# Optimization experiments

Measured on AMD Instinct MI355X. Metric: run time of the kernel, lower is better.

## Reference

```python
import jax, jax.numpy as jnp
import numpy as np

N_NODES = 50000
N_EDGES = 800000
IN_DIM = 64
HEADS = 8
OUT_DIM = 8
CLAMP = 5.0


def _xavier(key, shape, fan_in, fan_out):
    std = float(np.sqrt(2.0 / (fan_in + fan_out)))
    return jax.random.normal(key, shape, dtype=jnp.float32) * std


def setup_inputs() -> dict:
    key = jax.random.key(0)
    ks = jax.random.split(key, 12)
    H, D = HEADS, OUT_DIM
    hid = H * D
    x = jax.random.normal(ks[0], (N_NODES, IN_DIM), dtype=jnp.float32)
    edge_attr = jax.random.normal(ks[1], (N_EDGES, IN_DIM), dtype=jnp.float32)
    edge_index = jax.random.randint(ks[2], (2, N_EDGES), 0, N_NODES, dtype=jnp.int32)
    # Linear weights stored as [in, out] (torch stores [out, in]; math is x @ W)
    Wq = _xavier(ks[3], (IN_DIM, hid), IN_DIM, hid)
    bq = jnp.zeros((hid,), jnp.float32)
    Wk = _xavier(ks[4], (IN_DIM, hid), IN_DIM, hid)
    bk = jnp.zeros((hid,), jnp.float32)
    We = _xavier(ks[5], (IN_DIM, 2 * hid), IN_DIM, 2 * hid)
    be = jnp.zeros((2 * hid,), jnp.float32)
    Wv = _xavier(ks[6], (IN_DIM, hid), IN_DIM, hid)
    bv = jnp.zeros((hid,), jnp.float32)
    Aw = _xavier(ks[7], (D, H, 1), D * H, 1)
    VeRow = _xavier(ks[8], (D, H, D), D * H, D)
    return {"x": x, "edge_attr": edge_attr, "edge_index": edge_index,
            "Wq": Wq, "bq": bq, "Wk": Wk, "bk": bk, "We": We, "be": be,
            "Wv": Wv, "bv": bv, "Aw": Aw, "VeRow": VeRow}


def _signed_sqrt(x):
    # sqrt(relu(x)) - sqrt(relu(-x)) == sign(x)*sqrt(|x|), grad-safe form
    return jnp.sign(x) * jnp.sqrt(jnp.abs(x))


def _segment_softmax(src, index, num_segments):
    # src: [E, H, 1]; softmax over edges grouped by destination node
    m = jax.ops.segment_max(src, index, num_segments=num_segments)
    out = jnp.exp(src - m[index])
    s = jax.ops.segment_sum(out, index, num_segments=num_segments)
    return out / (s[index] + 1e-16)


def reference(x, edge_attr, edge_index, Wq, bq, Wk, bk, We, be, Wv, bv, Aw, VeRow):
    H, D = HEADS, OUT_DIM
    N = x.shape[0]
    src_idx, dst_idx = edge_index[0], edge_index[1]

    Q_h = (x @ Wq + bq).reshape(-1, H, D)
    K_h = (x @ Wk + bk).reshape(-1, H, D)
    V_h = (x @ Wv + bv).reshape(-1, H, D)
    E = (edge_attr @ We + be).reshape(-1, H, 2 * D)
    E_w, E_b = E[:, :, :D], E[:, :, D:]

    score = K_h[src_idx] + Q_h[dst_idx]          # [E, H, D]
    score = _signed_sqrt(score * E_w) + E_b
    score = jax.nn.relu(score)
    e_t = score                                   # [E, H, D]
    wE = e_t.reshape(e_t.shape[0], H * D)

    a = jnp.einsum('ehd,dhc->ehc', score, Aw)     # [E, H, 1]
    a = jnp.clip(a, -CLAMP, CLAMP)
    attn = _segment_softmax(a, dst_idx, N)        # [E, H, 1]

    msg = V_h[src_idx] * attn                     # [E, H, D]
    wV = jax.ops.segment_sum(msg, dst_idx, num_segments=N)
    rowV = jax.ops.segment_sum(e_t * attn, dst_idx, num_segments=N)
    rowV = jnp.einsum('nhd,dhc->nhc', rowV, VeRow)
    h_out = wV + rowV                             # [N, H, D]
    return h_out, wE
```

## Files before the change

### kernel.cpp

```cpp
#include <hip/hip_runtime.h>
#include <math.h>
#include <stdint.h>

#define N_NODES 50000
#define N_EDGES 800000
#define EDGE_BLOCKS 2500
#define TILES_PER_BLOCK 5
#define NCHUNK 256
#define CHN 196

#define GEMM_BLOCKS 2346
#define BPREP_BLOCKS 8
#define HIST_BLOCKS 3125

typedef __attribute__((ext_vector_type(8))) short short8;
typedef __attribute__((ext_vector_type(4))) float f32x4;

__device__ inline unsigned short bf16_rne(float x) {
    unsigned u = __float_as_uint(x);
    unsigned r = u + 0x7FFFu + ((u >> 16) & 1u);
    return (unsigned short)(r >> 16);
}
__device__ inline float bf16_to_f32(unsigned short h) {
    return __uint_as_float(((unsigned)h) << 16);
}

__global__ __launch_bounds__(256) void prep_kernel(
    const float* __restrict__ x,
    const float* __restrict__ Wq, const float* __restrict__ bq,
    const float* __restrict__ Wk, const float* __restrict__ bk,
    const float* __restrict__ Wv, const float* __restrict__ bv,
    const float* __restrict__ We,
    const int*   __restrict__ edge_index,
    float* __restrict__ Qo, float* __restrict__ Ko, float* __restrict__ Vo,
    unsigned short* __restrict__ Bg, int* __restrict__ counts)
{
    const int b = blockIdx.x;
    const int t = threadIdx.x;

    if (b >= GEMM_BLOCKS + BPREP_BLOCKS) {
        int e = (b - GEMM_BLOCKS - BPREP_BLOCKS) * 256 + t;
        if (e < N_EDGES) atomicAdd(&counts[edge_index[N_EDGES + e]], 1);
        return;
    }
    if (b >= GEMM_BLOCKS) {
        int tid = (b - GEMM_BLOCKS) * 256 + t;
        int k  = tid >> 5;
        int n4 = (tid & 31) * 4;
        float4 v4 = *(const float4*)&We[(size_t)k * 128 + n4];
        int c = k >> 5, qq = (k >> 3) & 3, jj = k & 7;
        float vv[4] = {v4.x, v4.y, v4.z, v4.w};
        #pragma unroll
        for (int u = 0; u < 4; u++) {
            int nn = n4 + u;
            int j  = nn >> 4;
            int ln = qq * 16 + (nn & 15);
            unsigned short hi = bf16_rne(vv[u]);
            unsigned short lo = bf16_rne(vv[u] - bf16_to_f32(hi));
            Bg[(j * 2 + c) * 512 + ln * 8 + jj] = hi;
            Bg[8192 + (j * 2 + c) * 512 + ln * 8 + jj] = lo;
        }
        return;
    }

    const int c  = b / 782;
    const int bx = b - c * 782;
    const float* W = (c == 0) ? Wq : (c == 1) ? Wk : Wv;
    const float* bb_ = (c == 0) ? bq : (c == 1) ? bk : bv;
    float* outp    = (c == 0) ? Qo : (c == 1) ? Ko : Vo;

    __shared__ float Xs[64][68];
    __shared__ float Ws[64][64];
    const int n0 = bx * 64;

    for (int i = 0; i < 4; i++) {
        int fi = t + i * 256;
        int row = fi >> 4, c4 = (fi & 15) * 4;
        float4 v = make_float4(0.f, 0.f, 0.f, 0.f);
        if (n0 + row < N_NODES) v = *(const float4*)&x[(size_t)(n0 + row) * 64 + c4];
        *(float4*)&Xs[row][c4] = v;
    }
    for (int i = 0; i < 4; i++) {
        int fi = t + i * 256;
        int row = fi >> 4, c4 = (fi & 15) * 4;
        *(float4*)&Ws[row][c4] = *(const float4*)&W[(size_t)row * 64 + c4];
    }
    __syncthreads();

    const int tx = t & 15, ty = t >> 4;
    float acc[4][4] = {};
    #pragma unroll
    for (int k4 = 0; k4 < 64; k4 += 4) {
        float4 xv[4], wv[4];
        #pragma unroll
        for (int r = 0; r < 4; r++) xv[r] = *(const float4*)&Xs[ty * 4 + r][k4];
        #pragma unroll
        for (int j = 0; j < 4; j++) wv[j] = *(const float4*)&Ws[k4 + j][tx * 4];
        #pragma unroll
        for (int r = 0; r < 4; r++) {
            acc[r][0] += xv[r].x * wv[0].x + xv[r].y * wv[1].x + xv[r].z * wv[2].x + xv[r].w * wv[3].x;
            acc[r][1] += xv[r].x * wv[0].y + xv[r].y * wv[1].y + xv[r].z * wv[2].y + xv[r].w * wv[3].y;
            acc[r][2] += xv[r].x * wv[0].z + xv[r].y * wv[1].z + xv[r].z * wv[2].z + xv[r].w * wv[3].z;
            acc[r][3] += xv[r].x * wv[0].w + xv[r].y * wv[1].w + xv[r].z * wv[2].w + xv[r].w * wv[3].w;
        }
    }
    float4 bv4 = *(const float4*)&bb_[tx * 4];
    #pragma unroll
    for (int r = 0; r < 4; r++) {
        int row = n0 + ty * 4 + r;
        if (row < N_NODES) {
            float4 o;
            o.x = acc[r][0] + bv4.x; o.y = acc[r][1] + bv4.y;
            o.z = acc[r][2] + bv4.z; o.w = acc[r][3] + bv4.w;
            *(float4*)&outp[(size_t)row * 64 + tx * 4] = o;
        }
    }
}

__global__ __launch_bounds__(256) void chunk_reduce_kernel(
    const int* __restrict__ counts, int* __restrict__ chunksum)
{
    __shared__ int red[256];
    const int c = blockIdx.x, t = threadIdx.x;
    int idx = c * CHN + t;
    int v = (t < CHN && idx < N_NODES) ? counts[idx] : 0;
    red[t] = v;
    __syncthreads();
    for (int s = 128; s > 0; s >>= 1) {
        if (t < s) red[t] += red[t + s];
        __syncthreads();
    }
    if (t == 0) chunksum[c] = red[0];
}

__global__ __launch_bounds__(256) void expand_kernel(
    const int* __restrict__ counts, const int* __restrict__ chunksum,
    int* __restrict__ cursor)
{
    __shared__ int shc[256];
    __shared__ int sh[256];
    const int c = blockIdx.x, t = threadIdx.x;
    shc[t] = chunksum[t];
    __syncthreads();
    for (int off = 1; off < 256; off <<= 1) {
        int v = (t >= off) ? shc[t - off] : 0;
        __syncthreads();
        shc[t] += v;
        __syncthreads();
    }
    int co = (c > 0) ? shc[c - 1] : 0;

    int idx = c * CHN + t;
    int own = (t < CHN && idx < N_NODES) ? counts[idx] : 0;
    sh[t] = own;
    __syncthreads();
    for (int off = 1; off < 256; off <<= 1) {
        int v = (t >= off) ? sh[t - off] : 0;
        __syncthreads();
        sh[t] += v;
        __syncthreads();
    }
    if (t < CHN && idx < N_NODES) cursor[idx] = sh[t] - own + co;
}

__global__ void scatter_kernel(const int* __restrict__ edge_index, int* __restrict__ cursor,
                               int4* __restrict__ es4)
{
    int e = blockIdx.x * 256 + threadIdx.x;
    if (e < N_EDGES) {
        int src = edge_index[e];
        int dst = edge_index[N_EDGES + e];
        int pos = atomicAdd(&cursor[dst], 1);
        es4[pos] = make_int4(e, src, dst, 0);
    }
}

__global__ __launch_bounds__(256, 3) void edge_kernel(
    const float* __restrict__ edge_attr,
    const int4*  __restrict__ es4,
    const unsigned short* __restrict__ Bg,
    const float* __restrict__ be,
    const float* __restrict__ Qws, const float* __restrict__ Kws,
    const float* __restrict__ Vws, const float* __restrict__ Aw,
    float* __restrict__ wE,
    float* __restrict__ WVacc, float* __restrict__ RVacc, float* __restrict__ Sacc)
{
    __shared__ __align__(16) unsigned short Bf[16384];
    __shared__ __align__(16) unsigned char  UB[17408];

    const int t    = threadIdx.x;
    const int lane = t & 63;
    const int w    = t >> 6;
    const int n    = lane & 15;
    const int q    = lane >> 4;
    const int d    = n & 7;
    const int h2   = lane >> 3;
    const int d2l  = lane & 7;

    float* kqw = (float*)(UB + w * 4352);

    for (int i = 0; i < 8; i++) {
        int o = t + i * 256;
        *(short8*)&Bf[o * 8] = *(const short8*)&Bg[o * 8];
    }
    float bev[8];
    #pragma unroll
    for (int j = 0; j < 8; j++) bev[j] = be[j * 16 + n];
    const float awv = Aw[d2l * 8 + h2];

    for (int it = 0; it < TILES_PER_BLOCK; it++) {
        const int tile  = blockIdx.x + it * EDGE_BLOCKS;
        const int wbase = tile * 64 + w * 16;

        __syncthreads();

        int eoA = es4[wbase + (lane & 15)].x;
        const float* arow = &edge_attr[(size_t)eoA * 64 + (lane >> 4) * 8];
        float4 a0 = *(const float4*)&arow[0];
        float4 a1 = *(const float4*)&arow[4];
        float4 a2 = *(const float4*)&arow[32];
        float4 a3 = *(const float4*)&arow[36];

        #pragma unroll
        for (int i = 0; i < 4; i++) {
            int idx = i * 64 + lane;
            int m   = idx >> 4;
            int c4  = (idx & 15) * 4;
            int4 es = es4[wbase + m];
            float4 kv = *(const float4*)&Kws[(size_t)es.y * 64 + c4];
            float4 qv = *(const float4*)&Qws[(size_t)es.z * 64 + c4];
            float4 o;
            o.x = kv.x + qv.x; o.y = kv.y + qv.y; o.z = kv.z + qv.z; o.w = kv.w + qv.w;
            *(float4*)&kqw[m * 68 + c4] = o;
        }

        float vbuf[16];
        int   dsts[16];
        #pragma unroll
        for (int k = 0; k < 16; k++) {
            int4 es = es4[wbase + k];
            dsts[k] = es.z;
            vbuf[k] = Vws[(size_t)es.y * 64 + lane];
        }

        float c0[8] = {a0.x, a0.y, a0.z, a0.w, a1.x, a1.y, a1.z, a1.w};
        float c1[8] = {a2.x, a2.y, a2.z, a2.w, a3.x, a3.y, a3.z, a3.w};
        short8 ah0, al0, ah1, al1;
        #pragma unroll
        for (int j = 0; j < 8; j++) {
            unsigned short hi = bf16_rne(c0[j]);
            ah0[j] = (short)hi;
            al0[j] = (short)bf16_rne(c0[j] - bf16_to_f32(hi));
        }
        #pragma unroll
        for (int j = 0; j < 8; j++) {
            unsigned short hi = bf16_rne(c1[j]);
            ah1[j] = (short)hi;
            al1[j] = (short)bf16_rne(c1[j] - bf16_to_f32(hi));
        }

        f32x4 acc[8];
        #pragma unroll
        for (int j = 0; j < 8; j++) acc[j] = (f32x4){0.f, 0.f, 0.f, 0.f};
        #pragma unroll
        for (int j = 0; j < 8; j++) {
            short8 bh0 = *(const short8*)&Bf[(j * 2 + 0) * 512 + lane * 8];
            short8 bh1 = *(const short8*)&Bf[(j * 2 + 1) * 512 + lane * 8];
            short8 bl0 = *(const short8*)&Bf[8192 + (j * 2 + 0) * 512 + lane * 8];
            short8 bl1 = *(const short8*)&Bf[8192 + (j * 2 + 1) * 512 + lane * 8];
            acc[j] = __builtin_amdgcn_mfma_f32_16x16x32_bf16(ah0, bh0, acc[j], 0, 0, 0);
            acc[j] = __builtin_amdgcn_mfma_f32_16x16x32_bf16(ah1, bh1, acc[j], 0, 0, 0);
            acc[j] = __builtin_amdgcn_mfma_f32_16x16x32_bf16(al0, bh0, acc[j], 0, 0, 0);
            acc[j] = __builtin_amdgcn_mfma_f32_16x16x32_bf16(al1, bh1, acc[j], 0, 0, 0);
            acc[j] = __builtin_amdgcn_mfma_f32_16x16x32_bf16(ah0, bl0, acc[j], 0, 0, 0);
            acc[j] = __builtin_amdgcn_mfma_f32_16x16x32_bf16(ah1, bl1, acc[j], 0, 0, 0);
        }

        #pragma unroll
        for (int j = 0; j < 8; j++) {
            #pragma unroll
            for (int r = 0; r < 4; r++) {
                int el = q * 4 + r;
                float Ev = acc[j][r] + bev[j];
                float pv = __shfl_xor(Ev, 8);
                float ew = (n < 8) ? Ev : pv;
                float eb = (n < 8) ? pv : Ev;
                float kq = kqw[el * 68 + j * 8 + d];
                float v  = kq * ew;
                float sc = copysignf(sqrtf(fabsf(v)), v) + eb;
                sc = fmaxf(sc, 0.0f);
                kqw[el * 68 + j * 8 + d] = sc;
            }
        }
        #pragma unroll
        for (int i = 0; i < 4; i++) {
            int el = i * 4 + q;
            int eo = es4[wbase + el].x;
            float4 o = *(const float4*)&kqw[el * 68 + n * 4];
            *(float4*)&wE[(size_t)eo * 64 + n * 4] = o;
        }

        float s_acc = 0.f, wvac = 0.f, rvac = 0.f;
        int cur = dsts[0];
        #pragma unroll
        for (int k = 0; k < 16; k++) {
            if (dsts[k] != cur) {
                atomicAdd(&WVacc[(size_t)cur * 64 + lane], wvac);
                atomicAdd(&RVacc[(size_t)cur * 64 + lane], rvac);
                if (d2l == 0) atomicAdd(&Sacc[cur * 8 + h2], s_acc);
                s_acc = 0.f; wvac = 0.f; rvac = 0.f;
                cur = dsts[k];
            }
            float sc = kqw[k * 68 + lane];
            float tv = sc * awv;
            tv += __shfl_xor(tv, 1); tv += __shfl_xor(tv, 2); tv += __shfl_xor(tv, 4);
            tv = fminf(fmaxf(tv, -5.0f), 5.0f);
            float ev = __expf(tv);
            s_acc += ev;
            wvac  += ev * vbuf[k];
            rvac  += ev * sc;
        }
        atomicAdd(&WVacc[(size_t)cur * 64 + lane], wvac);
        atomicAdd(&RVacc[(size_t)cur * 64 + lane], rvac);
        if (d2l == 0) atomicAdd(&Sacc[cur * 8 + h2], s_acc);
    }
}

__global__ __launch_bounds__(256) void finalize_kernel(
    const float* __restrict__ WVacc, const float* __restrict__ RVacc,
    const float* __restrict__ Sacc,  const float* __restrict__ VeRow,
    float* __restrict__ hout)
{
    const int t = threadIdx.x;
    const int lane = t & 63;
    const int w = t >> 6;
    const int node = blockIdx.x * 4 + w;
    const int h = lane >> 3, dd = lane & 7;
    float wv = WVacc[(size_t)node * 64 + lane];
    float rv = RVacc[(size_t)node * 64 + lane];
    float s  = Sacc[node * 8 + h];
    float rvt = 0.f;
    int gbase = lane & ~7;
    #pragma unroll
    for (int dk = 0; dk < 8; dk++) {
        float rvd = __shfl(rv, gbase + dk);
        rvt += rvd * VeRow[dk * 64 + h * 8 + dd];
    }
    hout[(size_t)node * 64 + lane] = (wv + rvt) / (s + 1e-16f);
}

extern "C" void kernel_launch(void* const* d_in, const int* in_sizes, int n_in,
                              void* d_out, int out_size, void* d_ws, size_t ws_size,
                              hipStream_t stream)
{
    const float* x         = (const float*)d_in[0];
    const float* edge_attr = (const float*)d_in[1];
    const int*   edge_index= (const int*)  d_in[2];
    const float* Wq = (const float*)d_in[3];  const float* bq = (const float*)d_in[4];
    const float* Wk = (const float*)d_in[5];  const float* bk = (const float*)d_in[6];
    const float* We = (const float*)d_in[7];  const float* be = (const float*)d_in[8];
    const float* Wv = (const float*)d_in[9];  const float* bv = (const float*)d_in[10];
    const float* Aw = (const float*)d_in[11]; const float* VeRow = (const float*)d_in[12];

    float* hout = (float*)d_out;
    float* wE   = hout + (size_t)N_NODES * 64;

    float* Q     = (float*)d_ws;
    float* K     = Q + (size_t)N_NODES * 64;
    float* V     = K + (size_t)N_NODES * 64;
    float* WVacc = V + (size_t)N_NODES * 64;
    float* RVacc = WVacc + (size_t)N_NODES * 64;
    float* Sacc  = RVacc + (size_t)N_NODES * 64;
    int* counts   = (int*)(Sacc + (size_t)N_NODES * 8);
    int* cursor   = counts + N_NODES;
    int* chunksum = cursor + N_NODES;
    unsigned short* Bg = (unsigned short*)(chunksum + NCHUNK);
    int4* es4     = (int4*)(((uintptr_t)(Bg + 16384) + 15) & ~(uintptr_t)15);

    hipMemsetAsync(counts, 0, N_NODES * sizeof(int), stream);
    hipMemsetAsync(WVacc, 0, (size_t)N_NODES * 136 * sizeof(float), stream);
    prep_kernel<<<GEMM_BLOCKS + BPREP_BLOCKS + HIST_BLOCKS, 256, 0, stream>>>(
        x, Wq, bq, Wk, bk, Wv, bv, We, edge_index, Q, K, V, Bg, counts);
    chunk_reduce_kernel<<<NCHUNK, 256, 0, stream>>>(counts, chunksum);
    expand_kernel<<<NCHUNK, 256, 0, stream>>>(counts, chunksum, cursor);
    scatter_kernel<<<(N_EDGES + 255) / 256, 256, 0, stream>>>(edge_index, cursor, es4);
    edge_kernel<<<EDGE_BLOCKS, 256, 0, stream>>>(edge_attr, es4, Bg, be,
                                                 Q, K, V, Aw, wE, WVacc, RVacc, Sacc);
    finalize_kernel<<<N_NODES / 4, 256, 0, stream>>>(WVacc, RVacc, Sacc, VeRow, hout);
}
```

Measured before the change: 675.3 us.

## Prefetch next tile's edge_attr, use packed bf16 converts, split redundant score work

The edge_attr rows for the next tile are now loaded right after the current tile's MFMA chain, so their global-memory latency overlaps the score epilogue instead of stalling at the start of each iteration. The hi/lo bf16 split of the A operand now uses the hardware v_cvt_pk_bf16_f32 instruction, replacing the software round-to-nearest-even bit manipulation. The epilogue is reorganised so lanes n<8 and n>=8 each handle different accumulator rows rather than both computing the same score, roughly halving the sqrt/copysign work. The cost is extra live registers for the prefetched float4s, which may add register pressure, plus one leftover dead code block.

```diff
diff --git a/kernel.cpp b/kernel.cpp
--- a/kernel.cpp
+++ b/kernel.cpp
@@ -23,6 +23,19 @@
 }
 __device__ inline float bf16_to_f32(unsigned short h) {
     return __uint_as_float(((unsigned)h) << 16);
+}
+
+__device__ inline unsigned cvtpk(float a, float b) {
+    unsigned r;
+    asm("v_cvt_pk_bf16_f32 %0, %1, %2" : "=v"(r) : "v"(a), "v"(b));
+    return r;
+}
+__device__ inline float pk_lo_f(unsigned w) { return __uint_as_float(w << 16); }
+__device__ inline float pk_hi_f(unsigned w) { return __uint_as_float(w & 0xFFFF0000u); }
+__device__ inline short8 pack4(unsigned w0, unsigned w1, unsigned w2, unsigned w3) {
+    union { unsigned u[4]; short8 s; } U;
+    U.u[0] = w0; U.u[1] = w1; U.u[2] = w2; U.u[3] = w3;
+    return U.s;
 }
 
 __global__ __launch_bounds__(256) void prep_kernel(
@@ -208,18 +221,27 @@
     for (int j = 0; j < 8; j++) bev[j] = be[j * 16 + n];
     const float awv = Aw[d2l * 8 + h2];
 
+    {
+        int wb0 = blockIdx.x * 64 + w * 16;
+        int eoA = es4[wb0 + (lane & 15)].x;
+        const float* arow = &edge_attr[(size_t)eoA * 64 + (lane >> 4) * 8];
+    }
+    float4 a0, a1, a2, a3;
+    {
+        int wb0 = blockIdx.x * 64 + w * 16;
+        int eoA = es4[wb0 + (lane & 15)].x;
+        const float* arow = &edge_attr[(size_t)eoA * 64 + (lane >> 4) * 8];
+        a0 = *(const float4*)&arow[0];
+        a1 = *(const float4*)&arow[4];
+        a2 = *(const float4*)&arow[32];
+        a3 = *(const float4*)&arow[36];
+    }
+
     for (int it = 0; it < TILES_PER_BLOCK; it++) {
         const int tile  = blockIdx.x + it * EDGE_BLOCKS;
         const int wbase = tile * 64 + w * 16;
 
         __syncthreads();
-
-        int eoA = es4[wbase + (lane & 15)].x;
-        const float* arow = &edge_attr[(size_t)eoA * 64 + (lane >> 4) * 8];
-        float4 a0 = *(const float4*)&arow[0];
-        float4 a1 = *(const float4*)&arow[4];
-        float4 a2 = *(const float4*)&arow[32];
-        float4 a3 = *(const float4*)&arow[36];
 
         #pragma unroll
         for (int i = 0; i < 4; i++) {
@@ -243,20 +265,26 @@
             vbuf[k] = Vws[(size_t)es.y * 64 + lane];
         }
 
-        float c0[8] = {a0.x, a0.y, a0.z, a0.w, a1.x, a1.y, a1.z, a1.w};
-        float c1[8] = {a2.x, a2.y, a2.z, a2.w, a3.x, a3.y, a3.z, a3.w};
         short8 ah0, al0, ah1, al1;
-        #pragma unroll
-        for (int j = 0; j < 8; j++) {
-            unsigned short hi = bf16_rne(c0[j]);
-            ah0[j] = (short)hi;
-            al0[j] = (short)bf16_rne(c0[j] - bf16_to_f32(hi));
-        }
-        #pragma unroll
-        for (int j = 0; j < 8; j++) {
-            unsigned short hi = bf16_rne(c1[j]);
-            ah1[j] = (short)hi;
-            al1[j] = (short)bf16_rne(c1[j] - bf16_to_f32(hi));
+        {
+            unsigned h0 = cvtpk(a0.x, a0.y), h1 = cvtpk(a0.z, a0.w);
+            unsigned h2_ = cvtpk(a1.x, a1.y), h3 = cvtpk(a1.z, a1.w);
+            unsigned l0 = cvtpk(a0.x - pk_lo_f(h0), a0.y - pk_hi_f(h0));
+            unsigned l1 = cvtpk(a0.z - pk_lo_f(h1), a0.w - pk_hi_f(h1));
+            unsigned l2 = cvtpk(a1.x - pk_lo_f(h2_), a1.y - pk_hi_f(h2_));
+            unsigned l3 = cvtpk(a1.z - pk_lo_f(h3), a1.w - pk_hi_f(h3));
+            ah0 = pack4(h0, h1, h2_, h3);
+            al0 = pack4(l0, l1, l2, l3);
+        }
+        {
+            unsigned h0 = cvtpk(a2.x, a2.y), h1 = cvtpk(a2.z, a2.w);
+            unsigned h2_ = cvtpk(a3.x, a3.y), h3 = cvtpk(a3.z, a3.w);
+            unsigned l0 = cvtpk(a2.x - pk_lo_f(h0), a2.y - pk_hi_f(h0));
+            unsigned l1 = cvtpk(a2.z - pk_lo_f(h1), a2.w - pk_hi_f(h1));
+            unsigned l2 = cvtpk(a3.x - pk_lo_f(h2_), a3.y - pk_hi_f(h2_));
+            unsigned l3 = cvtpk(a3.z - pk_lo_f(h3), a3.w - pk_hi_f(h3));
+            ah1 = pack4(h0, h1, h2_, h3);
+            al1 = pack4(l0, l1, l2, l3);
         }
 
         f32x4 acc[8];
@@ -276,15 +304,31 @@
             acc[j] = __builtin_amdgcn_mfma_f32_16x16x32_bf16(ah1, bl1, acc[j], 0, 0, 0);
         }
 
+        {
+            int tn  = (it + 1 < TILES_PER_BLOCK) ? tile + EDGE_BLOCKS : tile;
+            int wbn = tn * 64 + w * 16;
+            int eoN = es4[wbn + (lane & 15)].x;
+            const float* arn = &edge_attr[(size_t)eoN * 64 + (lane >> 4) * 8];
+            a0 = *(const float4*)&arn[0];
+            a1 = *(const float4*)&arn[4];
+            a2 = *(const float4*)&arn[32];
+            a3 = *(const float4*)&arn[36];
+        }
+
         #pragma unroll
         for (int j = 0; j < 8; j++) {
             #pragma unroll
-            for (int r = 0; r < 4; r++) {
-                int el = q * 4 + r;
-                float Ev = acc[j][r] + bev[j];
-                float pv = __shfl_xor(Ev, 8);
+            for (int rr = 0; rr < 2; rr++) {
+                float EvA = acc[j][rr]     + bev[j];
+                float EvB = acc[j][rr + 2] + bev[j];
+                float pvA = __shfl_xor(EvA, 8);
+                float pvB = __shfl_xor(EvB, 8);
+                int   r  = (n < 8) ? rr  : rr + 2;
+                float Ev = (n < 8) ? EvA : EvB;
+                float pv = (n < 8) ? pvA : pvB;
                 float ew = (n < 8) ? Ev : pv;
                 float eb = (n < 8) ? pv : Ev;
+                int el = q * 4 + r;
                 float kq = kqw[el * 68 + j * 8 + d];
                 float v  = kq * ew;
                 float sc = copysignf(sqrtf(fabsf(v)), v) + eb;
```

After: 651.5 us. 3.5% less time.
